# Kernel optimization log

Measured on AMD Instinct MI355X. Metric: run time of the kernel, lower is better.

Reference implementation:

```python
import jax, jax.numpy as jnp
import numpy as np

B, Q, K = 4, 512, 512
QUERY_SIZE = 512
KEY_SIZE = 512
NUM_HIDDENS = 256


def setup_inputs() -> dict:
    key = jax.random.key(0)
    k1, k2, k3, k4, k5 = jax.random.split(key, 5)
    queries = jax.random.normal(k1, (B, Q, 1, QUERY_SIZE), dtype=jnp.float32)
    keys = jax.random.normal(k2, (B, 1, K, KEY_SIZE), dtype=jnp.float32)
    # nn.Linear weights (bias=False); stored as (in, out) for einsum clarity
    W_q = jax.random.normal(k3, (QUERY_SIZE, NUM_HIDDENS), dtype=jnp.float32) * (1.0 / np.sqrt(QUERY_SIZE))
    W_k = jax.random.normal(k4, (KEY_SIZE, NUM_HIDDENS), dtype=jnp.float32) * (1.0 / np.sqrt(KEY_SIZE))
    w_v = jax.random.normal(k5, (NUM_HIDDENS,), dtype=jnp.float32) * (1.0 / np.sqrt(NUM_HIDDENS))
    return {"queries": queries, "keys": keys, "W_q": W_q, "W_k": W_k, "w_v": w_v}


def reference(queries, keys, W_q, W_k, w_v):
    # Project: queries (B,Q,1,Dq) -> (B,Q,1,H); keys (B,1,K,Dk) -> (B,1,K,H)
    q = jnp.einsum('bqod,dh->bqoh', queries, W_q)
    k = jnp.einsum('bokd,dh->bokh', keys, W_k)
    # Broadcast add -> (B,Q,K,H), tanh, reduce hidden via w_v -> (B,Q,K)
    features = jnp.tanh(q + k)
    scores = jnp.einsum('bqkh,h->bqk', features, w_v)
    return scores
```

## Files before the change

kernel.cpp:

```cpp
#include <hip/hip_runtime.h>
#include <hip/hip_bf16.h>

#define HH 256
#define DD 512
#define MM 2048
#define CSCALE 2.8853900817779268f

typedef __bf16 bf16x8 __attribute__((ext_vector_type(8)));
typedef float floatx4 __attribute__((ext_vector_type(4)));

__global__ __launch_bounds__(256) void prep_kernel(
    const float* __restrict__ Wq, const float* __restrict__ Wk,
    const float* __restrict__ wv,
    const float* __restrict__ queries, const float* __restrict__ keys,
    __bf16* __restrict__ Wt, __bf16* __restrict__ Xbf,
    float* __restrict__ wv2, float* __restrict__ sumWp)
{
  const int bx = blockIdx.x;
  if (bx < 256) {
    const int mat  = bx >> 7;
    const int tile = bx & 127;
    const int kt = tile & 15;
    const int nt = tile >> 4;
    const float* __restrict__ W = mat ? Wk : Wq;
    __bf16* __restrict__ Wo = Wt + (size_t)mat * HH * DD;
    __shared__ float lds[32][33];
    const int i = threadIdx.x >> 5;
    const int j = threadIdx.x & 31;
    const int k0 = kt * 32, n0 = nt * 32;
#pragma unroll
    for (int p = 0; p < 4; ++p)
      lds[i + p * 8][j] = W[(k0 + i + p * 8) * HH + n0 + j];
    __syncthreads();
#pragma unroll
    for (int p = 0; p < 4; ++p) {
      const int n = i + p * 8;
      Wo[(n0 + n) * DD + k0 + j] = (__bf16)(lds[j][n] * CSCALE);
    }
  } else if (bx == 256) {
    __shared__ float red[256];
    const int t = threadIdx.x;
    float w = wv[t];
    wv2[t] = -2.0f * w;
    red[t] = w;
    __syncthreads();
    for (int s = 128; s > 0; s >>= 1) {
      if (t < s) red[t] += red[t + s];
      __syncthreads();
    }
    if (t == 0) *sumWp = red[0];
  } else {
    const int blk = bx - 257;
    const size_t dst = (size_t)blk * 2048 + threadIdx.x * 8;
    const float* __restrict__ src =
        (blk < 512) ? (queries + dst) : (keys + dst - (size_t)1048576);
    float4 a = *(const float4*)(src);
    float4 b = *(const float4*)(src + 4);
    bf16x8 v;
    v[0] = (__bf16)a.x; v[1] = (__bf16)a.y; v[2] = (__bf16)a.z; v[3] = (__bf16)a.w;
    v[4] = (__bf16)b.x; v[5] = (__bf16)b.y; v[6] = (__bf16)b.z; v[7] = (__bf16)b.w;
    *(bf16x8*)(Xbf + dst) = v;
  }
}

__global__ __launch_bounds__(256, 4) void proj_kernel(
    const __bf16* __restrict__ Xbf, const __bf16* __restrict__ Wt,
    float* __restrict__ eqp, __bf16* __restrict__ ekb)
{
  const int w    = threadIdx.x >> 6;
  const int lane = threadIdx.x & 63;
  const int quad = lane >> 4;
  const int r    = lane & 15;
  const int tw = w & 1;
  const int ks = w >> 1;
  const bool is_k = (blockIdx.z != 0);
  const __bf16* __restrict__ X  = Xbf + (is_k ? (size_t)1048576 : 0);
  const __bf16* __restrict__ Wb = Wt + (is_k ? (size_t)HH * DD : 0);

  const int m0 = blockIdx.x * 32 + tw * 16;
  const int n0 = blockIdx.y * 32;

  floatx4 acc0 = {0.f, 0.f, 0.f, 0.f};
  floatx4 acc1 = {0.f, 0.f, 0.f, 0.f};
  const __bf16* arow = X + (size_t)(m0 + r) * DD + ks * 256 + quad * 8;
  const __bf16* b0   = Wb + (size_t)(n0 + r) * DD + ks * 256 + quad * 8;
  const __bf16* b1   = b0 + 16 * DD;

#pragma unroll
  for (int kk = 0; kk < 256; kk += 32) {
    bf16x8 af  = *(const bf16x8*)(arow + kk);
    bf16x8 bf0 = *(const bf16x8*)(b0 + kk);
    bf16x8 bf1 = *(const bf16x8*)(b1 + kk);
    acc0 = __builtin_amdgcn_mfma_f32_16x16x32_bf16(af, bf0, acc0, 0, 0, 0);
    acc1 = __builtin_amdgcn_mfma_f32_16x16x32_bf16(af, bf1, acc1, 0, 0, 0);
  }

  __shared__ float part[2][64][9];
  if (ks == 1) {
#pragma unroll
    for (int i = 0; i < 4; ++i) {
      part[tw][lane][i]     = acc0[i];
      part[tw][lane][4 + i] = acc1[i];
    }
  }
  __syncthreads();
  if (ks == 0) {
#pragma unroll
    for (int i = 0; i < 4; ++i) {
      acc0[i] += part[tw][lane][i];
      acc1[i] += part[tw][lane][4 + i];
    }
    const int mrow = m0 + quad * 4;
    if (!is_k) {
#pragma unroll
      for (int i = 0; i < 4; ++i) {
        eqp[(size_t)(mrow + i) * HH + n0 + r] =
            __builtin_amdgcn_exp2f(acc0[i]);
        eqp[(size_t)(mrow + i) * HH + n0 + 16 + r] =
            __builtin_amdgcn_exp2f(acc1[i]);
      }
    } else {
      const int na = n0 + r, nb = n0 + 16 + r;
#pragma unroll
      for (int i = 0; i < 4; ++i) {
        const int m = mrow + i;
        ekb[(((size_t)(m >> 4) * 64 + (na >> 2)) * 16 + (m & 15)) * 4 + (na & 3)] =
            (__bf16)__builtin_amdgcn_exp2f(acc0[i]);
        ekb[(((size_t)(m >> 4) * 64 + (nb >> 2)) * 16 + (m & 15)) * 4 + (nb & 3)] =
            (__bf16)__builtin_amdgcn_exp2f(acc1[i]);
      }
    }
  }
}

__device__ __forceinline__ float quad_term(
    float ek0, float ek1, float ek2, float ek3,
    float4 e, float4 w, float acc)
{
  float u0 = fmaf(e.x, ek0, 1.0f);
  float u1 = fmaf(e.y, ek1, 1.0f);
  float u2 = fmaf(e.z, ek2, 1.0f);
  float u3 = fmaf(e.w, ek3, 1.0f);
  float p01 = u0 * u1;
  float p23 = u2 * u3;
  float n01 = fmaf(w.y, u0, w.x * u1);
  float n23 = fmaf(w.w, u2, w.z * u3);
  float N   = fmaf(n23, p01, n01 * p23);
  float r   = __builtin_amdgcn_rcpf(p01 * p23);
  return fmaf(N, r, acc);
}

__global__ __launch_bounds__(512, 8) void score_kernel(
    const float* __restrict__ eqp, const uint2* __restrict__ ekb,
    const float* __restrict__ wv2, const float* __restrict__ sumWp,
    float* __restrict__ out)
{
  __shared__ __align__(16) float eqs[2][4][128];
  __shared__ __align__(16) float wvs[2][128];
  __shared__ __align__(16) float part[4][256];

  const int tid = threadIdx.x;
  const int t   = tid & 255;
  const int hb  = tid >> 8;
  const int b   = blockIdx.z;
  const int k   = blockIdx.x * 256 + t;
  const int q0  = blockIdx.y * 4;

  {
    const int i0 = tid, i1 = tid + 512;
    eqs[0][(i0 >> 7) & 3][i0 & 127] =
        eqp[(size_t)(b * 512 + q0 + ((i0 >> 7) & 3)) * HH + (i0 & 127)];
    eqs[1][(i1 >> 7) & 3][i1 & 127] =
        eqp[(size_t)(b * 512 + q0 + ((i1 >> 7) & 3)) * HH + 128 + (i1 & 127)];
    if (tid < 256) wvs[tid >> 7][tid & 127] = wv2[tid];
  }
  __syncthreads();

  const int m = b * 512 + k;
  const uint2* __restrict__ kptr =
      ekb + ((size_t)(m >> 4) * 64 + hb * 32) * 16 + (m & 15);

  float acc0 = 0.f, acc1 = 0.f, acc2 = 0.f, acc3 = 0.f;

  for (int c = 0; c < 8; ++c) {
    uint2 kb[4];
#pragma unroll
    for (int i = 0; i < 4; ++i)
      kb[i] = kptr[(c * 4 + i) * 16];
#pragma unroll
    for (int i = 0; i < 4; ++i) {
      const int hq = c * 4 + i;
      float ek0 = __uint_as_float(kb[i].x << 16);
      float ek1 = __uint_as_float(kb[i].x & 0xffff0000u);
      float ek2 = __uint_as_float(kb[i].y << 16);
      float ek3 = __uint_as_float(kb[i].y & 0xffff0000u);
      float4 w4 = *(const float4*)&wvs[hb][hq * 4];
      acc0 = quad_term(ek0, ek1, ek2, ek3, *(const float4*)&eqs[hb][0][hq * 4], w4, acc0);
      acc1 = quad_term(ek0, ek1, ek2, ek3, *(const float4*)&eqs[hb][1][hq * 4], w4, acc1);
      acc2 = quad_term(ek0, ek1, ek2, ek3, *(const float4*)&eqs[hb][2][hq * 4], w4, acc2);
      acc3 = quad_term(ek0, ek1, ek2, ek3, *(const float4*)&eqs[hb][3][hq * 4], w4, acc3);
    }
  }

  if (hb == 1) {
    part[0][t] = acc0; part[1][t] = acc1;
    part[2][t] = acc2; part[3][t] = acc3;
  }
  __syncthreads();
  if (hb == 0) {
    const float sumW = *sumWp;
    float* obase = out + ((size_t)(b * 512 + q0)) * 512 + blockIdx.x * 256 + t;
    obase[0]    = sumW + acc0 + part[0][t];
    obase[512]  = sumW + acc1 + part[1][t];
    obase[1024] = sumW + acc2 + part[2][t];
    obase[1536] = sumW + acc3 + part[3][t];
  }
}

extern "C" void kernel_launch(void* const* d_in, const int* in_sizes, int n_in,
                              void* d_out, int out_size, void* d_ws, size_t ws_size,
                              hipStream_t stream) {
  (void)in_sizes; (void)n_in; (void)out_size; (void)ws_size;
  const float* queries = (const float*)d_in[0];
  const float* Keys    = (const float*)d_in[1];
  const float* Wq      = (const float*)d_in[2];
  const float* Wk      = (const float*)d_in[3];
  const float* wv      = (const float*)d_in[4];
  float* out = (float*)d_out;

  char* ws = (char*)d_ws;
  __bf16* Wt    = (__bf16*)ws;
  float*  wv2   = (float*)(ws + (512 << 10));
  float*  sumWp = (float*)(ws + (513 << 10));
  __bf16* Xbf   = (__bf16*)(ws + (1 << 20));
  float*  eqp   = (float*)(ws + (5ull << 20));
  __bf16* ekb   = (__bf16*)(ws + (7ull << 20));

  prep_kernel<<<dim3(1281), 256, 0, stream>>>(
      Wq, Wk, wv, queries, Keys, Wt, Xbf, wv2, sumWp);
  proj_kernel<<<dim3(64, 8, 2), 256, 0, stream>>>(Xbf, Wt, eqp, ekb);
  score_kernel<<<dim3(2, 128, 4), 512, 0, stream>>>(
      eqp, (const uint2*)ekb, wv2, sumWp, out);
}
```

Baseline: 107.5 us.

## Store exp(k) as fp32 and drop LDS staging and hidden split in score kernel

The key-side exponentials are now stored as fp32 float4 groups instead of packed bf16, which removes the unpack shifts in the score loop. The score kernel goes from 512-thread blocks that split the hidden dimension in two to 256-thread blocks that loop over all 256 hidden units. Query exponentials and the weights are read straight from global memory (uniform, cacheable) instead of being staged in LDS, which also removes the LDS partial-sum reduction and both barriers. The cost is twice the bytes for the key buffer, a longer serial loop per thread, and fewer threads per block.

```diff
diff --git a/kernel.cpp b/kernel.cpp
--- a/kernel.cpp
+++ b/kernel.cpp
@@ -65,7 +65,7 @@
 
 __global__ __launch_bounds__(256, 4) void proj_kernel(
     const __bf16* __restrict__ Xbf, const __bf16* __restrict__ Wt,
-    float* __restrict__ eqp, __bf16* __restrict__ ekb)
+    float* __restrict__ eqp, float* __restrict__ ekf)
 {
   const int w    = threadIdx.x >> 6;
   const int lane = threadIdx.x & 63;
@@ -124,23 +124,22 @@
 #pragma unroll
       for (int i = 0; i < 4; ++i) {
         const int m = mrow + i;
-        ekb[(((size_t)(m >> 4) * 64 + (na >> 2)) * 16 + (m & 15)) * 4 + (na & 3)] =
-            (__bf16)__builtin_amdgcn_exp2f(acc0[i]);
-        ekb[(((size_t)(m >> 4) * 64 + (nb >> 2)) * 16 + (m & 15)) * 4 + (nb & 3)] =
-            (__bf16)__builtin_amdgcn_exp2f(acc1[i]);
+        ekf[((size_t)(m >> 4) * 64 + (na >> 2)) * 64 + (m & 15) * 4 + (na & 3)] =
+            __builtin_amdgcn_exp2f(acc0[i]);
+        ekf[((size_t)(m >> 4) * 64 + (nb >> 2)) * 64 + (m & 15) * 4 + (nb & 3)] =
+            __builtin_amdgcn_exp2f(acc1[i]);
       }
     }
   }
 }
 
 __device__ __forceinline__ float quad_term(
-    float ek0, float ek1, float ek2, float ek3,
-    float4 e, float4 w, float acc)
-{
-  float u0 = fmaf(e.x, ek0, 1.0f);
-  float u1 = fmaf(e.y, ek1, 1.0f);
-  float u2 = fmaf(e.z, ek2, 1.0f);
-  float u3 = fmaf(e.w, ek3, 1.0f);
+    float4 ek, float4 e, float4 w, float acc)
+{
+  float u0 = fmaf(e.x, ek.x, 1.0f);
+  float u1 = fmaf(e.y, ek.y, 1.0f);
+  float u2 = fmaf(e.z, ek.z, 1.0f);
+  float u3 = fmaf(e.w, ek.w, 1.0f);
   float p01 = u0 * u1;
   float p23 = u2 * u3;
   float n01 = fmaf(w.y, u0, w.x * u1);
@@ -150,71 +149,50 @@
   return fmaf(N, r, acc);
 }
 
-__global__ __launch_bounds__(512, 8) void score_kernel(
-    const float* __restrict__ eqp, const uint2* __restrict__ ekb,
+__global__ __launch_bounds__(256, 4) void score_kernel(
+    const float* __restrict__ eqp, const float4* __restrict__ ekf,
     const float* __restrict__ wv2, const float* __restrict__ sumWp,
     float* __restrict__ out)
 {
-  __shared__ __align__(16) float eqs[2][4][128];
-  __shared__ __align__(16) float wvs[2][128];
-  __shared__ __align__(16) float part[4][256];
-
-  const int tid = threadIdx.x;
-  const int t   = tid & 255;
-  const int hb  = tid >> 8;
-  const int b   = blockIdx.z;
-  const int k   = blockIdx.x * 256 + t;
-  const int q0  = blockIdx.y * 4;
-
-  {
-    const int i0 = tid, i1 = tid + 512;
-    eqs[0][(i0 >> 7) & 3][i0 & 127] =
-        eqp[(size_t)(b * 512 + q0 + ((i0 >> 7) & 3)) * HH + (i0 & 127)];
-    eqs[1][(i1 >> 7) & 3][i1 & 127] =
-        eqp[(size_t)(b * 512 + q0 + ((i1 >> 7) & 3)) * HH + 128 + (i1 & 127)];
-    if (tid < 256) wvs[tid >> 7][tid & 127] = wv2[tid];
-  }
-  __syncthreads();
+  const int t  = threadIdx.x;
+  const int b  = blockIdx.z;
+  const int k  = blockIdx.x * 256 + t;
+  const int q0 = blockIdx.y * 4;
+
+  const float* __restrict__ e0p = eqp + (size_t)(b * 512 + q0) * HH;
+  const float* __restrict__ e1p = e0p + HH;
+  const float* __restrict__ e2p = e0p + 2 * HH;
+  const float* __restrict__ e3p = e0p + 3 * HH;
 
   const int m = b * 512 + k;
-  const uint2* __restrict__ kptr =
-      ekb + ((size_t)(m >> 4) * 64 + hb * 32) * 16 + (m & 15);
+  const float4* __restrict__ kp =
+      ekf + (size_t)(m >> 4) * 1024 + (m & 15);
 
   float acc0 = 0.f, acc1 = 0.f, acc2 = 0.f, acc3 = 0.f;
 
-  for (int c = 0; c < 8; ++c) {
-    uint2 kb[4];
+  for (int c = 0; c < 16; ++c) {
+    float4 kb[4];
 #pragma unroll
     for (int i = 0; i < 4; ++i)
-      kb[i] = kptr[(c * 4 + i) * 16];
+      kb[i] = kp[i * 16];
+    kp += 64;
 #pragma unroll
     for (int i = 0; i < 4; ++i) {
-      const int hq = c * 4 + i;
-      float ek0 = __uint_as_float(kb[i].x << 16);
-      float ek1 = __uint_as_float(kb[i].x & 0xffff0000u);
-      float ek2 = __uint_as_float(kb[i].y << 16);
-      float ek3 = __uint_as_float(kb[i].y & 0xffff0000u);
-      float4 w4 = *(const float4*)&wvs[hb][hq * 4];
-      acc0 = quad_term(ek0, ek1, ek2, ek3, *(const float4*)&eqs[hb][0][hq * 4], w4, acc0);
-      acc1 = quad_term(ek0, ek1, ek2, ek3, *(const float4*)&eqs[hb][1][hq * 4], w4, acc1);
-      acc2 = quad_term(ek0, ek1, ek2, ek3, *(const float4*)&eqs[hb][2][hq * 4], w4, acc2);
-      acc3 = quad_term(ek0, ek1, ek2, ek3, *(const float4*)&eqs[hb][3][hq * 4], w4, acc3);
-    }
-  }
-
-  if (hb == 1) {
-    part[0][t] = acc0; part[1][t] = acc1;
-    part[2][t] = acc2; part[3][t] = acc3;
-  }
-  __syncthreads();
-  if (hb == 0) {
-    const float sumW = *sumWp;
-    float* obase = out + ((size_t)(b * 512 + q0)) * 512 + blockIdx.x * 256 + t;
-    obase[0]    = sumW + acc0 + part[0][t];
-    obase[512]  = sumW + acc1 + part[1][t];
-    obase[1024] = sumW + acc2 + part[2][t];
-    obase[1536] = sumW + acc3 + part[3][t];
-  }
+      const int h4 = c * 16 + i * 4;
+      float4 w4 = *(const float4*)(wv2 + h4);
+      acc0 = quad_term(kb[i], *(const float4*)(e0p + h4), w4, acc0);
+      acc1 = quad_term(kb[i], *(const float4*)(e1p + h4), w4, acc1);
+      acc2 = quad_term(kb[i], *(const float4*)(e2p + h4), w4, acc2);
+      acc3 = quad_term(kb[i], *(const float4*)(e3p + h4), w4, acc3);
+    }
+  }
+
+  const float sumW = *sumWp;
+  float* obase = out + (size_t)(b * 512 + q0) * 512 + blockIdx.x * 256 + t;
+  obase[0]    = sumW + acc0;
+  obase[512]  = sumW + acc1;
+  obase[1024] = sumW + acc2;
+  obase[1536] = sumW + acc3;
 }
 
 extern "C" void kernel_launch(void* const* d_in, const int* in_sizes, int n_in,
@@ -234,11 +212,11 @@
   float*  sumWp = (float*)(ws + (513 << 10));
   __bf16* Xbf   = (__bf16*)(ws + (1 << 20));
   float*  eqp   = (float*)(ws + (5ull << 20));
-  __bf16* ekb   = (__bf16*)(ws + (7ull << 20));
+  float*  ekf   = (float*)(ws + (8ull << 20));
 
   prep_kernel<<<dim3(1281), 256, 0, stream>>>(
       Wq, Wk, wv, queries, Keys, Wt, Xbf, wv2, sumWp);
-  proj_kernel<<<dim3(64, 8, 2), 256, 0, stream>>>(Xbf, Wt, eqp, ekb);
-  score_kernel<<<dim3(2, 128, 4), 512, 0, stream>>>(
-      eqp, (const uint2*)ekb, wv2, sumWp, out);
-}
+  proj_kernel<<<dim3(64, 8, 2), 256, 0, stream>>>(Xbf, Wt, eqp, ekf);
+  score_kernel<<<dim3(2, 128, 4), 256, 0, stream>>>(
+      eqp, (const float4*)ekf, wv2, sumWp, out);
+}
```

After: 108.7 us. Within noise of the previous version (+1.1%).
